# Optimization experiments

Hardware: AMD Instinct MI355X
Metric: run time of the kernel (lower is better)

The kernel has to match this reference:

```python
import jax, jax.numpy as jnp
import numpy as np

N, C, K, PARTS = 32, 256, 8192, 16
MAX_INIT = -100.0  # matches torch new_full((n,c,P), -100.0) with include_self=True


def setup_inputs() -> dict:
    key = jax.random.key(0)
    k1, k2, k3 = jax.random.split(key, 3)
    feats = jax.random.normal(k1, (N, C, K), dtype=jnp.float32)
    part_labels = jax.random.randint(k2, (K,), 0, PARTS, dtype=jnp.int64)
    valid_mask = jax.random.bernoulli(k3, 0.5, (N, K))
    return {"feats": feats, "part_labels": part_labels, "valid_mask": valid_mask}


def reference(feats, part_labels, valid_mask):
    n, c, k = feats.shape
    labels = part_labels.astype(jnp.int32)  # [k]
    vm = valid_mask.astype(feats.dtype)     # [n, k]

    # masked features for the mean branch (max branch uses raw feats, as in torch)
    valid_feat = feats * vm[:, None, :]      # [n, c, k]

    # scatter-add sum of valid features per part: [n, c, P]
    pooled_sum = jnp.zeros((n, c, PARTS), feats.dtype).at[:, :, labels].add(valid_feat)
    # scatter-add count of valid anchors per part: [n, P]
    pooled_count = jnp.zeros((n, PARTS), feats.dtype).at[:, labels].add(vm)
    # scatter-max over raw feats (unmasked, include_self with -100 init): [n, c, P]
    pooled_max = jnp.full((n, c, PARTS), MAX_INIT, feats.dtype).at[:, :, labels].max(feats)
    # anchors per part, independent of sample/mask: [P]
    patch_count = jnp.zeros((PARTS,), feats.dtype).at[labels].add(1.0)

    pooled_mean = pooled_sum / jnp.maximum(pooled_count, 1.0)[:, None, :]
    pooled_max = jnp.where(patch_count > 0, pooled_max, jnp.zeros_like(pooled_max))
    return pooled_mean + pooled_max  # [n, c, P]
```

## Files before the change

### kernel.cpp

```cpp
#include <hip/hip_runtime.h>

#define NN 32
#define CC 256
#define KK 8192
#define PARTS 16
#define TPB 256
#define PSTR 640
#define CH 16
#define NCH (CC / CH)
#define MAX_INIT (-100.0f)

typedef unsigned int uint32;
typedef unsigned short u16;

__device__ __forceinline__ uint32 swz(uint32 g) {
    return g ^ (((g >> 3) ^ (g >> 6)) & 7u);
}


__global__ __launch_bounds__(TPB) void prep_kernel(const int* __restrict__ labels,
                                                   const int* __restrict__ vm,
                                                   int* __restrict__ pcount,
                                                   u16* __restrict__ permbase,
                                                   uint32* __restrict__ bmask) {
    const int t = threadIdx.x;
    const int blk = blockIdx.x;

    if (blk >= PARTS) {
        const int n = blk - PARTS;
        const int4* v4 = (const int4*)(vm + (size_t)n * KK) + t * 8;
        uint32 bits = 0;
#pragma unroll
        for (int j = 0; j < 8; ++j) {
            int4 v = v4[j];
            bits |= (uint32)(v.x != 0) << (4 * j) | (uint32)(v.y != 0) << (4 * j + 1) |
                    (uint32)(v.z != 0) << (4 * j + 2) | (uint32)(v.w != 0) << (4 * j + 3);
        }
        bmask[n * 256 + t] = bits;
        return;
    }

    const int p = blk;
    __shared__ __align__(16) u16 sperm[PSTR];
    __shared__ u16 wtot[4];
    __shared__ uint32 stot;
    const int w = t >> 6;
    const int lane = t & 63;

    int4 lv[8];
    const int4* l4 = (const int4*)labels + t * 8;
#pragma unroll
    for (int j = 0; j < 8; ++j) lv[j] = l4[j];

    uint32 c = 0;
#pragma unroll
    for (int j = 0; j < 8; ++j) {
        c += ((lv[j].x & 15) == p) + ((lv[j].y & 15) == p) +
             ((lv[j].z & 15) == p) + ((lv[j].w & 15) == p);
    }
    uint32 inc = c;
#pragma unroll
    for (int s = 1; s < 64; s <<= 1) {
        uint32 o = __shfl_up(inc, s, 64);
        if (lane >= s) inc += o;
    }
    if (lane == 63) wtot[w] = (u16)inc;
    __syncthreads();
    uint32 base = inc - c;
    for (int ww = 0; ww < w; ++ww) base += wtot[ww];
    if (t == TPB - 1) stot = base + c;

    uint32 pos = base;
#pragma unroll
    for (int j = 0; j < 8; ++j) {
        int la[4] = {lv[j].x, lv[j].y, lv[j].z, lv[j].w};
#pragma unroll
        for (int cc = 0; cc < 4; ++cc) {
            if ((la[cc] & 15) == p) {
                if (pos < PSTR) sperm[pos] = (u16)(t * 32 + j * 4 + cc);
                ++pos;
            }
        }
    }
    __syncthreads();

    const uint32 total = stot;
    const u16 fill = (u16)((total ? (sperm[0] & 0x1fffu) : 0u) | 0x4000u);
    for (uint32 q = total + t; q < PSTR; q += TPB) sperm[q] = fill;
    if (t == 0) pcount[p] = (int)total;
    __syncthreads();

    const uint4* src = (const uint4*)sperm;
    uint4* dst = (uint4*)(permbase + p * PSTR);
    for (int i = t; i < PSTR * 2 / 16; i += TPB) dst[i] = src[i];
}

__global__ __launch_bounds__(TPB, 2) void pool_kernel(const float* __restrict__ feats,
                                                      const u16* __restrict__ permbase,
                                                      const int* __restrict__ pcount,
                                                      const uint32* __restrict__ bmask,
                                                      float* __restrict__ out) {
    __shared__ uint32 srow[2 * KK];
    __shared__ uint32 smask[256];
    const int t = threadIdx.x;
    const int blk = blockIdx.x;
    const int n = blk / NCH;
    const int c0 = (blk % NCH) * CH;
    const int w = t >> 6;
    const int lane = t & 63;
    const int g = t >> 4;
    const int l = t & 15;

    uint32 woff[8];
#pragma unroll
    for (int i = 0; i < 8; ++i) {
        uint32 r = (uint32)(w * 8 + i) * 64u + (uint32)lane;
        woff[i] = swz(r) * 4u;
    }

    auto STAGE = [&](int buf, int r) {
        const uint32* frow = (const uint32*)(feats + (size_t)(n * CC + c0 + r) * KK);
#pragma unroll
        for (int i = 0; i < 8; ++i) {
            __builtin_amdgcn_global_load_lds(
                (const __attribute__((address_space(1))) unsigned int*)(frow + woff[i]),
                (__attribute__((address_space(3))) unsigned int*)&srow[buf * KK + (w * 8 + i) * 256],
                16, 0, 0);
        }
    };

    STAGE(0, 0);
    STAGE(1, 1);

    smask[t] = bmask[n * 256 + t];

    uint32 pk[20];
    {
        const uint4* pb4 = (const uint4*)(permbase + g * PSTR + l * 40);
#pragma unroll
        for (int j = 0; j < 5; ++j) {
            uint4 q = pb4[j];
            pk[j * 4 + 0] = q.x;
            pk[j * 4 + 1] = q.y;
            pk[j * 4 + 2] = q.z;
            pk[j * 4 + 3] = q.w;
        }
    }
    __syncthreads();

    uint32 ga[40];
    float gm[40];
    int cnt = 0;
#pragma unroll
    for (int i = 0; i < 40; ++i) {
        uint32 e = (pk[i >> 1] >> (16 * (i & 1))) & 0xffffu;
        uint32 k = e & 0x1fffu;
        uint32 valid = (e & 0x4000u) ? 0u : ((smask[k >> 5] >> (k & 31u)) & 1u);
        uint32 pos = swz(k >> 2);
        ga[i] = pos * 16u + (k & 3u) * 4u;
        gm[i] = valid ? 1.0f : 0.0f;
        cnt += (int)valid;
    }
#pragma unroll
    for (int m = 1; m < 16; m <<= 1) cnt += __shfl_xor(cnt, m, 16);
    const float cv = fmaxf((float)cnt, 1.0f);
    const int ph = pcount[g];

    for (int r = 0; r < CH; ++r) {
        if (r < CH - 1) {
            asm volatile("s_waitcnt vmcnt(8)" ::: "memory");
        } else {
            asm volatile("s_waitcnt vmcnt(0)" ::: "memory");
        }
        __builtin_amdgcn_s_barrier();

        const char* rowb = (const char*)&srow[(r & 1) * KK];
        float rs0 = 0.0f, rs1 = 0.0f, rs2 = 0.0f, rs3 = 0.0f;
        float rm0 = MAX_INIT, rm1 = MAX_INIT, rm2 = MAX_INIT, rm3 = MAX_INIT;
#pragma unroll
        for (int i = 0; i < 40; i += 4) {
            float f0 = *(const float*)(rowb + ga[i]);
            float f1 = *(const float*)(rowb + ga[i + 1]);
            float f2 = *(const float*)(rowb + ga[i + 2]);
            float f3 = *(const float*)(rowb + ga[i + 3]);
            rm0 = fmaxf(rm0, f0);
            rs0 = fmaf(f0, gm[i], rs0);
            rm1 = fmaxf(rm1, f1);
            rs1 = fmaf(f1, gm[i + 1], rs1);
            rm2 = fmaxf(rm2, f2);
            rs2 = fmaf(f2, gm[i + 2], rs2);
            rm3 = fmaxf(rm3, f3);
            rs3 = fmaf(f3, gm[i + 3], rs3);
        }
        float rs = (rs0 + rs1) + (rs2 + rs3);
        float rm = fmaxf(fmaxf(rm0, rm1), fmaxf(rm2, rm3));
#pragma unroll
        for (int m = 1; m < 16; m <<= 1) {
            rs += __shfl_xor(rs, m, 16);
            rm = fmaxf(rm, __shfl_xor(rm, m, 16));
        }
        if (l == 0)
            out[(size_t)(n * CC + c0 + r) * PARTS + g] = rs / cv + (ph > 0 ? rm : 0.0f);

        __builtin_amdgcn_s_barrier();
        if (r + 2 < CH) STAGE(r & 1, r + 2);
    }
}

extern "C" void kernel_launch(void* const* d_in, const int* in_sizes, int n_in,
                              void* d_out, int out_size, void* d_ws, size_t ws_size,
                              hipStream_t stream) {
    const float* feats  = (const float*)d_in[0];
    const int*   labels = (const int*)d_in[1];
    const int*   vm     = (const int*)d_in[2];
    float* out = (float*)d_out;

    int*    pcount   = (int*)d_ws;
    u16*    permbase = (u16*)((char*)d_ws + 64);
    uint32* bmask    = (uint32*)((char*)d_ws + 24576);

    prep_kernel<<<PARTS + NN, TPB, 0, stream>>>(labels, vm, pcount, permbase, bmask);
    pool_kernel<<<NN * NCH, TPB, 0, stream>>>(feats, permbase, pcount, bmask, out);
}
```

Measured before the change: 54.95 us.

## Stage rows through registers into single LDS buffer to raise occupancy

Replaces the double-buffered direct global-to-LDS row staging with register-staged prefetch (global load into float4 registers, then write into a single LDS row buffer). This halves LDS use so four blocks can be resident per CU, and halves rows per block so twice as many blocks launch. Gather addresses are packed two per 32-bit register and validity flags into two bitmasks, which frees VGPRs for the extra occupancy. The cost is an extra barrier per row, register traffic for staging, and each block now loads its per-part permutation and mask setup for only 8 rows, so that setup is amortised over less work.

```diff
diff --git a/kernel.cpp b/kernel.cpp
--- a/kernel.cpp
+++ b/kernel.cpp
@@ -6,7 +6,7 @@
 #define PARTS 16
 #define TPB 256
 #define PSTR 640
-#define CH 16
+#define CH 8
 #define NCH (CC / CH)
 #define MAX_INIT (-100.0f)
 
@@ -95,12 +95,12 @@
     for (int i = t; i < PSTR * 2 / 16; i += TPB) dst[i] = src[i];
 }
 
-__global__ __launch_bounds__(TPB, 2) void pool_kernel(const float* __restrict__ feats,
+__global__ __launch_bounds__(TPB, 4) void pool_kernel(const float* __restrict__ feats,
                                                       const u16* __restrict__ permbase,
                                                       const int* __restrict__ pcount,
                                                       const uint32* __restrict__ bmask,
                                                       float* __restrict__ out) {
-    __shared__ uint32 srow[2 * KK];
+    __shared__ uint32 srow[KK];
     __shared__ uint32 smask[256];
     const int t = threadIdx.x;
     const int blk = blockIdx.x;
@@ -111,27 +111,28 @@
     const int g = t >> 4;
     const int l = t & 15;
 
-    uint32 woff[8];
+    uint32 soff[8];
 #pragma unroll
     for (int i = 0; i < 8; ++i) {
-        uint32 r = (uint32)(w * 8 + i) * 64u + (uint32)lane;
-        woff[i] = swz(r) * 4u;
-    }
-
-    auto STAGE = [&](int buf, int r) {
-        const uint32* frow = (const uint32*)(feats + (size_t)(n * CC + c0 + r) * KK);
-#pragma unroll
-        for (int i = 0; i < 8; ++i) {
-            __builtin_amdgcn_global_load_lds(
-                (const __attribute__((address_space(1))) unsigned int*)(frow + woff[i]),
-                (__attribute__((address_space(3))) unsigned int*)&srow[buf * KK + (w * 8 + i) * 256],
-                16, 0, 0);
-        }
-    };
-
-    STAGE(0, 0);
-    STAGE(1, 1);
-
+        uint32 q = (uint32)(w * 8 + i) * 64u + (uint32)lane;
+        soff[i] = swz(q);
+    }
+
+    float4 stg[8];
+#define LOADR(r)                                                                  \
+    do {                                                                          \
+        const float4* s_ = (const float4*)(feats + (size_t)(n * CC + c0 + (r)) * KK); \
+        _Pragma("unroll")                                                         \
+        for (int i_ = 0; i_ < 8; ++i_) stg[i_] = s_[soff[i_]];                    \
+    } while (0)
+#define WRITEL()                                                                  \
+    do {                                                                          \
+        _Pragma("unroll")                                                         \
+        for (int i_ = 0; i_ < 8; ++i_)                                            \
+            *(float4*)&srow[((w * 8 + i_) * 64 + lane) * 4] = stg[i_];            \
+    } while (0)
+
+    LOADR(0);
     smask[t] = bmask[n * 256 + t];
 
     uint32 pk[20];
@@ -146,20 +147,32 @@
             pk[j * 4 + 3] = q.w;
         }
     }
-    __syncthreads();
-
-    uint32 ga[40];
-    float gm[40];
+    WRITEL();
+    LOADR(1);
+    asm volatile("s_waitcnt lgkmcnt(0)" ::: "memory");
+    __builtin_amdgcn_s_barrier();
+    __builtin_amdgcn_sched_barrier(0);
+
+    uint32 pa[20];
+    uint32 vb0 = 0, vb1 = 0;
     int cnt = 0;
 #pragma unroll
-    for (int i = 0; i < 40; ++i) {
-        uint32 e = (pk[i >> 1] >> (16 * (i & 1))) & 0xffffu;
-        uint32 k = e & 0x1fffu;
-        uint32 valid = (e & 0x4000u) ? 0u : ((smask[k >> 5] >> (k & 31u)) & 1u);
-        uint32 pos = swz(k >> 2);
-        ga[i] = pos * 16u + (k & 3u) * 4u;
-        gm[i] = valid ? 1.0f : 0.0f;
-        cnt += (int)valid;
+    for (int j = 0; j < 20; ++j) {
+        uint32 two = pk[j];
+        uint32 packed = 0;
+#pragma unroll
+        for (int h = 0; h < 2; ++h) {
+            uint32 e = (two >> (16 * h)) & 0xffffu;
+            uint32 k = e & 0x1fffu;
+            uint32 valid = (e & 0x4000u) ? 0u : ((smask[k >> 5] >> (k & 31u)) & 1u);
+            uint32 ba = swz(k >> 2) * 16u + (k & 3u) * 4u;
+            packed |= ba << (16 * h);
+            int i = j * 2 + h;
+            if (i < 32) vb0 |= valid << i;
+            else        vb1 |= valid << (i - 32);
+            cnt += (int)valid;
+        }
+        pa[j] = packed;
     }
 #pragma unroll
     for (int m = 1; m < 16; m <<= 1) cnt += __shfl_xor(cnt, m, 16);
@@ -167,30 +180,27 @@
     const int ph = pcount[g];
 
     for (int r = 0; r < CH; ++r) {
-        if (r < CH - 1) {
-            asm volatile("s_waitcnt vmcnt(8)" ::: "memory");
-        } else {
-            asm volatile("s_waitcnt vmcnt(0)" ::: "memory");
-        }
-        __builtin_amdgcn_s_barrier();
-
-        const char* rowb = (const char*)&srow[(r & 1) * KK];
+        const char* rowb = (const char*)srow;
         float rs0 = 0.0f, rs1 = 0.0f, rs2 = 0.0f, rs3 = 0.0f;
         float rm0 = MAX_INIT, rm1 = MAX_INIT, rm2 = MAX_INIT, rm3 = MAX_INIT;
 #pragma unroll
-        for (int i = 0; i < 40; i += 4) {
-            float f0 = *(const float*)(rowb + ga[i]);
-            float f1 = *(const float*)(rowb + ga[i + 1]);
-            float f2 = *(const float*)(rowb + ga[i + 2]);
-            float f3 = *(const float*)(rowb + ga[i + 3]);
+        for (int j = 0; j < 20; j += 2) {
+            uint32 p0 = pa[j];
+            uint32 p1 = pa[j + 1];
+            float f0 = *(const float*)(rowb + (p0 & 0xffffu));
+            float f1 = *(const float*)(rowb + (p0 >> 16));
+            float f2 = *(const float*)(rowb + (p1 & 0xffffu));
+            float f3 = *(const float*)(rowb + (p1 >> 16));
+            uint32 va = (j * 2 < 32) ? vb0 : vb1;
+            uint32 vbb = ((j + 1) * 2 < 32) ? vb0 : vb1;
             rm0 = fmaxf(rm0, f0);
-            rs0 = fmaf(f0, gm[i], rs0);
+            rs0 += ((va >> ((j * 2) & 31)) & 1u) ? f0 : 0.0f;
             rm1 = fmaxf(rm1, f1);
-            rs1 = fmaf(f1, gm[i + 1], rs1);
+            rs1 += ((va >> ((j * 2 + 1) & 31)) & 1u) ? f1 : 0.0f;
             rm2 = fmaxf(rm2, f2);
-            rs2 = fmaf(f2, gm[i + 2], rs2);
+            rs2 += ((vbb >> ((j * 2 + 2) & 31)) & 1u) ? f2 : 0.0f;
             rm3 = fmaxf(rm3, f3);
-            rs3 = fmaf(f3, gm[i + 3], rs3);
+            rs3 += ((vbb >> ((j * 2 + 3) & 31)) & 1u) ? f3 : 0.0f;
         }
         float rs = (rs0 + rs1) + (rs2 + rs3);
         float rm = fmaxf(fmaxf(rm0, rm1), fmaxf(rm2, rm3));
@@ -203,8 +213,17 @@
             out[(size_t)(n * CC + c0 + r) * PARTS + g] = rs / cv + (ph > 0 ? rm : 0.0f);
 
         __builtin_amdgcn_s_barrier();
-        if (r + 2 < CH) STAGE(r & 1, r + 2);
-    }
+        __builtin_amdgcn_sched_barrier(0);
+        if (r + 1 < CH) {
+            WRITEL();
+            if (r + 2 < CH) LOADR(r + 2);
+            asm volatile("s_waitcnt lgkmcnt(0)" ::: "memory");
+            __builtin_amdgcn_s_barrier();
+            __builtin_amdgcn_sched_barrier(0);
+        }
+    }
+#undef LOADR
+#undef WRITEL
 }
 
 extern "C" void kernel_launch(void* const* d_in, const int* in_sizes, int n_in,
```

Result: slower. 139.0 us (+152.9%).
